# Kernel tuning notes

Hardware: AMD Instinct MI355X
Metric: run time of the kernel (lower is better)

The kernel has to match this reference:

```python
import jax, jax.numpy as jnp
import numpy as np

T = 1024
DIMS = 256


def setup_inputs() -> dict:
    key = jax.random.key(0)
    k1, k2, k3, k4 = jax.random.split(key, 4)
    k = jax.random.normal(k1, (T, DIMS), dtype=jnp.float32)
    v = jax.random.normal(k2, (T, DIMS), dtype=jnp.float32)
    time_first = jax.random.normal(k3, (DIMS,), dtype=jnp.float32)
    # time_decay must be negative so exp(decay * (i+1-j)) does not overflow
    # for lags up to T (torch.randn init would overflow at T=1024).
    time_decay = -(jax.random.uniform(k4, (DIMS,), dtype=jnp.float32) * 4.0 + 0.1)
    return {"k": k, "v": v, "time_first": time_first, "time_decay": time_decay}


def reference(k, v, time_first, time_decay):
    T_, D = k.shape
    idx = jnp.arange(T_)
    mask = idx[:, None] >= idx[None, :]                      # [T,T] causal (tril)
    # tri[i,j] = i+1-j on/below diagonal, 0 above (matches torch .tril())
    tri = jnp.where(mask, (idx[:, None] + 1 - idx[None, :]), 0).astype(k.dtype)
    # t[i,j,d] = exp(time_decay[d] * tri[i,j]) * mask[i,j]   # [T,T,D] ~1GB
    t = jnp.exp(time_decay[None, None, :] * tri[:, :, None]) * mask[:, :, None]
    kx = jnp.exp(k)                                          # [T,D]
    vx = v * kx                                              # [T,D]
    kxr = jnp.einsum('ijd,jd->id', t, kx)                    # decay-weighted causal sums
    vxr = jnp.einsum('ijd,jd->id', t, vx)
    tf = jnp.exp(time_first)                                 # [D]
    # Faithful to source: numerator uses kxr, denominator uses vxr (as written).
    vxx = vx * tf + kxr
    kxx = kx * tf + vxr
    return vxx / kxx
```

## Files before the change

### kernel.cpp

```cpp
#include <hip/hip_runtime.h>


constexpr int T = 1024;
constexpr int D = 256;
constexpr int L = 16;

__global__ __launch_bounds__(64) void wkv_scan_kernel(
    const float* __restrict__ k, const float* __restrict__ v,
    const float* __restrict__ time_first, const float* __restrict__ time_decay,
    float* __restrict__ out)
{
    const int d    = blockIdx.x;
    const int lane = threadIdx.x;

    const float td = time_decay[d];
    const float wd = __expf(td);
    const float tf = __expf(time_first[d]);

    const int base = lane * L;

    float kx[L], vx[L];
    float bk = 0.f, bv = 0.f;
#pragma unroll
    for (int j = 0; j < L; ++j) {
        const float kk = k[(base + j) * D + d];
        const float vv = v[(base + j) * D + d];
        const float e  = __expf(kk);
        kx[j] = e;
        vx[j] = vv * e;
        bk = wd * (e + bk);
        bv = wd * (vx[j] + bv);
    }

    float f = __expf(td * (float)L);
#pragma unroll
    for (int o = 1; o < 64; o <<= 1) {
        const float pk = __shfl_up(bk, o);
        const float pv = __shfl_up(bv, o);
        if (lane >= o) {
            bk = fmaf(f, pk, bk);
            bv = fmaf(f, pv, bv);
        }
        f = f * f;
    }

    float sk = __shfl_up(bk, 1);
    float sv = __shfl_up(bv, 1);
    if (lane == 0) { sk = 0.f; sv = 0.f; }

#pragma unroll
    for (int j = 0; j < L; ++j) {
        sk = wd * (kx[j] + sk);
        sv = wd * (vx[j] + sv);
        const float num = fmaf(vx[j], tf, sk);
        const float den = fmaf(kx[j], tf, sv);
        out[(base + j) * D + d] = num * __builtin_amdgcn_rcpf(den);
    }
}

extern "C" void kernel_launch(void* const* d_in, const int* in_sizes, int n_in,
                              void* d_out, int out_size, void* d_ws, size_t ws_size,
                              hipStream_t stream) {
    const float* k  = (const float*)d_in[0];
    const float* v  = (const float*)d_in[1];
    const float* tf = (const float*)d_in[2];
    const float* td = (const float*)d_in[3];
    float* out = (float*)d_out;

    dim3 grid(D);
    dim3 block(64);
    wkv_scan_kernel<<<grid, block, 0, stream>>>(k, v, tf, td, out);
}
```

Measured before the change: 11.55 us.

## Group 16 channels per block and scan chunk carries via shared memory

Reorganizes the kernel so each 1024-thread block handles 16 adjacent channels, with threads split across time chunks. Adjacent threads now read adjacent channels, which is meant to coalesce global loads and stores. Chunk carries are transposed through shared memory so that one wavefront per channel can do the cross-chunk shuffle scan. The trade-off is that the grid shrinks to 16 blocks, which reduces how many compute units are used, and two block barriers are added.

New measurement: 12.78 us (median of 2 runs). 10.7% more time.

```diff
diff --git a/kernel.cpp b/kernel.cpp
--- a/kernel.cpp
+++ b/kernel.cpp
@@ -1,28 +1,34 @@
 #include <hip/hip_runtime.h>
 
 
-constexpr int T = 1024;
-constexpr int D = 256;
-constexpr int L = 16;
+constexpr int T  = 1024;
+constexpr int D  = 256;
+constexpr int GD = 16;
+constexpr int RT = 16;
+constexpr int NCH = T / RT;
+constexpr int NTH = NCH * GD;
 
-__global__ __launch_bounds__(64) void wkv_scan_kernel(
+__global__ __launch_bounds__(NTH) void wkv_scan_kernel(
     const float* __restrict__ k, const float* __restrict__ v,
     const float* __restrict__ time_first, const float* __restrict__ time_decay,
     float* __restrict__ out)
 {
-    const int d    = blockIdx.x;
-    const int lane = threadIdx.x;
+    __shared__ float cK[NCH][GD + 1];
+    __shared__ float cV[NCH][GD + 1];
+
+    const int t  = threadIdx.x;
+    const int dd = t & (GD - 1);
+    const int c  = t >> 4;
+    const int d  = blockIdx.x * GD + dd;
 
     const float td = time_decay[d];
     const float wd = __expf(td);
-    const float tf = __expf(time_first[d]);
 
-    const int base = lane * L;
-
-    float kx[L], vx[L];
+    const int base = c * RT;
+    float kx[RT], vx[RT];
     float bk = 0.f, bv = 0.f;
 #pragma unroll
-    for (int j = 0; j < L; ++j) {
+    for (int j = 0; j < RT; ++j) {
         const float kk = k[(base + j) * D + d];
         const float vv = v[(base + j) * D + d];
         const float e  = __expf(kk);
@@ -31,25 +37,42 @@
         bk = wd * (e + bk);
         bv = wd * (vx[j] + bv);
     }
+    cK[c][dd] = bk;
+    cV[c][dd] = bv;
+    __syncthreads();
 
-    float f = __expf(td * (float)L);
+    {
+        const int w    = t >> 6;
+        const int lane = t & 63;
+        const float tdw = time_decay[blockIdx.x * GD + w];
+
+        float sbk = cK[lane][w];
+        float sbv = cV[lane][w];
+
+        float f = __expf(tdw * (float)RT);
 #pragma unroll
-    for (int o = 1; o < 64; o <<= 1) {
-        const float pk = __shfl_up(bk, o);
-        const float pv = __shfl_up(bv, o);
-        if (lane >= o) {
-            bk = fmaf(f, pk, bk);
-            bv = fmaf(f, pv, bv);
+        for (int o = 1; o < 64; o <<= 1) {
+            const float pk = __shfl_up(sbk, o);
+            const float pv = __shfl_up(sbv, o);
+            if (lane >= o) {
+                sbk = fmaf(f, pk, sbk);
+                sbv = fmaf(f, pv, sbv);
+            }
+            f = f * f;
         }
-        f = f * f;
+        float ek = __shfl_up(sbk, 1);
+        float ev = __shfl_up(sbv, 1);
+        if (lane == 0) { ek = 0.f; ev = 0.f; }
+        cK[lane][w] = ek;
+        cV[lane][w] = ev;
     }
+    __syncthreads();
 
-    float sk = __shfl_up(bk, 1);
-    float sv = __shfl_up(bv, 1);
-    if (lane == 0) { sk = 0.f; sv = 0.f; }
-
+    const float tf = __expf(time_first[d]);
+    float sk = cK[c][dd];
+    float sv = cV[c][dd];
 #pragma unroll
-    for (int j = 0; j < L; ++j) {
+    for (int j = 0; j < RT; ++j) {
         sk = wd * (kx[j] + sk);
         sv = wd * (vx[j] + sv);
         const float num = fmaf(vx[j], tf, sk);
@@ -67,7 +90,7 @@
     const float* td = (const float*)d_in[3];
     float* out = (float*)d_out;
 
-    dim3 grid(D);
-    dim3 block(64);
+    dim3 grid(D / GD);
+    dim3 block(NTH);
     wkv_scan_kernel<<<grid, block, 0, stream>>>(k, v, tf, td, out);
 }
```
